# Performance work log

Measured on AMD Instinct MI355X. Metric: run time of the kernel, lower is better.

## Reference

```python
import jax, jax.numpy as jnp
import numpy as np

B, T, D, H, DH, COUT, PRED, K, DFF = 16, 512, 512, 8, 64, 7, 96, 16, 2048
LOW_FREQ = 1
LN_EPS = 1e-5


def _next_fast_len(n):
    while True:
        m = n
        for p in (2, 3, 5):
            while m % p == 0:
                m //= p
        if m == 1:
            return n
        n += 1


def conv1d_fft(f, g, axis=1):
    # FFT cross-correlation, matching torch conv1d_fft (roll + tail slice)
    N = f.shape[axis]
    M = g.shape[axis]
    L = _next_fast_len(N + M - 1)
    Ff = jnp.fft.rfft(f, n=L, axis=axis)
    Fg = jnp.fft.rfft(g, n=L, axis=axis)
    out = jnp.fft.irfft(Ff * jnp.conj(Fg), n=L, axis=axis)
    out = jnp.roll(out, -1, axis=axis)
    return jax.lax.slice_in_dim(out, L - N, L, axis=axis)


def es_weights(sw, T_):
    alpha = jax.nn.sigmoid(sw)                       # (h,1)
    powers = jnp.arange(T_, dtype=jnp.float32)       # (T,)
    init_w = alpha ** (powers + 1.0)                 # (h,T)
    w = (1.0 - alpha) * alpha ** powers[::-1]        # (h,T)
    return init_w.T[None, :, :, None], w.T[None, :, :, None]  # (1,T,h,1)


def exponential_smoothing(values, v0, sw, aux_values=None):
    b, t, h, d = values.shape
    init_w, w = es_weights(sw, t)
    out = init_w * v0 + conv1d_fft(values, w, axis=1)
    if aux_values is not None:
        alpha = jax.nn.sigmoid(sw).reshape(1, 1, h, 1)
        aux_w = w / jnp.maximum(1.0 - alpha, 1e-6) * alpha
        out = out + conv1d_fft(aux_values, aux_w, axis=1)
    return out


def fourier_extrapolate(x, pred_len, k, low_freq=LOW_FREQ):
    b, t, d = x.shape
    x_freq = jnp.fft.rfft(x, axis=1)                 # (b, t//2+1, d)
    hi_end = x_freq.shape[1] - 1 if t % 2 == 0 else x_freq.shape[1]
    x_freq_high = x_freq[:, low_freq:hi_end]
    k_ = k if (k is not None and k < t // 2) else max(1, hi_end - low_freq)
    k_ = min(k_, x_freq_high.shape[1])
    mag = jnp.abs(x_freq_high).transpose(0, 2, 1)    # (b,d,F)
    _, idx = jax.lax.top_k(mag, k_)                  # (b,d,k)
    idx = idx.transpose(0, 2, 1) + low_freq          # (b,k,d)
    x_topk = jnp.take_along_axis(x_freq, idx, axis=1)
    freqs = jnp.fft.rfftfreq(t).astype(jnp.float32)
    f_topk = jnp.take_along_axis(
        jnp.broadcast_to(freqs[None, :, None], (b, freqs.shape[0], d)), idx, axis=1)
    x_ex = jnp.concatenate([x_topk, jnp.conj(x_topk)], axis=1)   # (b,2k,d)
    f_ex = jnp.concatenate([f_topk, -f_topk], axis=1)
    tt = jnp.arange(t + pred_len, dtype=jnp.float32)[None, None, :, None]
    amp = (jnp.abs(x_ex) / t)[:, :, None, :]
    phase = jnp.angle(x_ex)[:, :, None, :]
    x_time = amp * jnp.cos(2.0 * jnp.pi * f_ex[:, :, None, :] * tt + phase)
    return x_time.sum(axis=1)                        # (b, t+pred_len, d)


def layer_norm(x, g, b, eps=LN_EPS):
    mu = x.mean(-1, keepdims=True)
    var = ((x - mu) ** 2).mean(-1, keepdims=True)
    return (x - mu) / jnp.sqrt(var + eps) * g + b


def _forward(res, level, Wi, bi, z0, v0_g, sw_g, Wo, bo, W1, W2,
             g1, b1_ln, g2, b2_ln, Wg, bg, Ws, bs, v0_l, sw_l):
    b, t, _ = res.shape
    # season block
    season = fourier_extrapolate(res, PRED, K)               # (b, t+PRED, d)
    res1 = res - season[:, :t]
    # growth block
    v = (res1 @ Wi.T + bi).reshape(b, t, H, DH)
    v = jnp.concatenate([jnp.broadcast_to(z0[None, None], (b, 1, H, DH)), v], axis=1)
    diffs = v[:, 1:] - v[:, :-1]                             # (b,t,H,DH)
    sm = exponential_smoothing(diffs, v0_g, sw_g)
    gr = jnp.concatenate([jnp.broadcast_to(v0_g, (b, 1, H, DH)), sm], axis=1)
    growth = gr.reshape(b, t + 1, H * DH) @ Wo.T + bo        # (b,t+1,d)
    # residual path
    h = layer_norm(res1 - growth[:, 1:], g1, b1_ln)
    ff = jax.nn.relu(h @ W1.T) @ W2.T
    h = layer_norm(h + ff, g2, b2_ln)
    # level block
    gp = growth[:, 1:t + 1] @ Wg.T + bg                      # (b,t,COUT)
    sp = season[:, :t] @ Ws.T + bs
    es_in = (level - sp)[..., None]                          # (b,t,COUT,1)
    lvl = exponential_smoothing(es_in, v0_l, sw_l, aux_values=gp[..., None])[..., 0]
    return h, lvl, growth, season


def setup_inputs() -> dict:
    key = jax.random.key(0)
    ks = jax.random.split(key, 20)
    s = 0.02
    return {
        "res": jax.random.normal(ks[0], (B, T, D), jnp.float32),
        "level": jax.random.normal(ks[1], (B, T, COUT), jnp.float32),
        "Wi": jax.random.normal(ks[2], (H * DH, D), jnp.float32) * s,
        "bi": jnp.zeros((H * DH,), jnp.float32),
        "z0": jax.random.normal(ks[3], (H, DH), jnp.float32),
        "v0_g": jax.random.normal(ks[4], (1, 1, H, DH), jnp.float32),
        "sw_g": jax.random.normal(ks[5], (H, 1), jnp.float32),
        "Wo": jax.random.normal(ks[6], (D, H * DH), jnp.float32) * s,
        "bo": jnp.zeros((D,), jnp.float32),
        "W1": jax.random.normal(ks[7], (DFF, D), jnp.float32) * s,
        "W2": jax.random.normal(ks[8], (D, DFF), jnp.float32) * s,
        "g1": jnp.ones((D,), jnp.float32),
        "b1_ln": jnp.zeros((D,), jnp.float32),
        "g2": jnp.ones((D,), jnp.float32),
        "b2_ln": jnp.zeros((D,), jnp.float32),
        "Wg": jax.random.normal(ks[9], (COUT, D), jnp.float32) * s,
        "bg": jnp.zeros((COUT,), jnp.float32),
        "Ws": jax.random.normal(ks[10], (COUT, D), jnp.float32) * s,
        "bs": jnp.zeros((COUT,), jnp.float32),
        "v0_l": jax.random.normal(ks[11], (1, 1, COUT, 1), jnp.float32),
        "sw_l": jax.random.normal(ks[12], (COUT, 1), jnp.float32),
    }


def reference(res, level, Wi, bi, z0, v0_g, sw_g, Wo, bo, W1, W2,
              g1, b1_ln, g2, b2_ln, Wg, bg, Ws, bs, v0_l, sw_l):
    return _forward(res, level, Wi, bi, z0, v0_g, sw_g, Wo, bo, W1, W2,
                    g1, b1_ln, g2, b2_ln, Wg, bg, Ws, bs, v0_l, sw_l)
```

## Files before the change

kernel.cpp:

```cpp
#include <hip/hip_runtime.h>
#include <math.h>

#define Bn 16
#define Tn 512
#define Dn 512
#define COUTn 7
#define PREDn 96

using f32x4 = __attribute__((ext_vector_type(4))) float;
using bf16x8 = __attribute__((ext_vector_type(8))) __bf16;

__device__ __forceinline__ unsigned short f2b(float f) {
  unsigned int u = __float_as_uint(f);
  u += 0x7fff + ((u >> 16) & 1);
  return (unsigned short)(u >> 16);
}

__device__ __forceinline__ void gld16(const void* g, void* l) {
  __builtin_amdgcn_global_load_lds(
      (const __attribute__((address_space(1))) void*)g,
      (__attribute__((address_space(3))) void*)l, 16, 0, 0);
}

__global__ __launch_bounds__(256) void cvt_bf16(
    const float* __restrict__ in, unsigned short* __restrict__ out, int n) {
  int i = (blockIdx.x * 256 + threadIdx.x) * 4;
  if (i + 3 < n) {
    float4 v = *reinterpret_cast<const float4*>(&in[i]);
    ushort4 o;
    o.x = f2b(v.x); o.y = f2b(v.y); o.z = f2b(v.z); o.w = f2b(v.w);
    *reinterpret_cast<ushort4*>(&out[i]) = o;
  }
}

__global__ __launch_bounds__(256) void twiddle_init2(
    unsigned short* __restrict__ twc_b, unsigned short* __restrict__ tws_b,
    double* __restrict__ tabw, float* __restrict__ c512,
    float* __restrict__ s512) {
  int idx = blockIdx.x * 256 + threadIdx.x;
  int k = idx >> 9, t = idx & 511;
  int m = (k * t) & 511;
  double ang = (double)m * (M_PI / 256.0);
  twc_b[idx] = f2b((float)cos(ang));
  tws_b[idx] = f2b((float)sin(ang));
  if (idx < 512) {
    double a2 = (double)idx * (M_PI / 256.0);
    c512[idx] = (float)cos(a2);
    s512[idx] = (float)sin(a2);
    tabw[2 * idx] = cos(a2);
    tabw[2 * idx + 1] = -sin(a2);
  }
}

__global__ __launch_bounds__(256) void transpose_cvt(
    const float* __restrict__ res, unsigned short* __restrict__ resT) {
  __shared__ unsigned short tile[64][65];
  int b = blockIdx.z;
  int t0 = blockIdx.y * 64, d0 = blockIdx.x * 64;
  int tid = threadIdx.x;
  int c = tid & 63, r4 = (tid >> 6) * 16;
#pragma unroll
  for (int i = 0; i < 16; ++i) {
    int t = t0 + r4 + i;
    tile[r4 + i][c] = f2b(res[((size_t)(b * 512 + t)) * 512 + d0 + c]);
  }
  __syncthreads();
#pragma unroll
  for (int i = 0; i < 16; ++i) {
    int d = d0 + r4 + i;
    resT[((size_t)(b * 512 + d)) * 512 + t0 + c] = tile[c][r4 + i];
  }
}

__global__ __launch_bounds__(256) void screen_mfma(
    const unsigned short* __restrict__ twc_b,
    const unsigned short* __restrict__ tws_b,
    const unsigned short* __restrict__ resT, float* __restrict__ mag) {
  __shared__ unsigned short lAc[2][2048];
  __shared__ unsigned short lAs[2][2048];
  __shared__ unsigned short lB[2][4096];
  int tid = threadIdx.x;
  int wv = tid >> 6, lane = tid & 63;
  int b = blockIdx.z;
  int k0 = blockIdx.y * 64;
  int d0 = blockIdx.x * 128;

  int rA = wv * 16 + (lane >> 2);
  int rB0 = wv * 32 + (lane >> 2);
  int rB1 = rB0 + 16;
  int kk = (lane & 3) * 8;
  int kkA = kk ^ (((rA >> 1) & 3) << 3);
  int kkB0 = kk ^ (((rB0 >> 1) & 3) << 3);
  int kkB1 = kk ^ (((rB1 >> 1) & 3) << 3);
  const unsigned short* ac = twc_b + (size_t)(k0 + rA) * 512 + kkA;
  const unsigned short* as = tws_b + (size_t)(k0 + rA) * 512 + kkA;
  const unsigned short* bb0 = resT + ((size_t)(b * 512 + d0 + rB0)) * 512 + kkB0;
  const unsigned short* bb1 = resT + ((size_t)(b * 512 + d0 + rB1)) * 512 + kkB1;

  int frow = lane & 15, fk = (lane >> 4) * 8;
  int ia[4], ib[2];
#pragma unroll
  for (int i = 0; i < 4; ++i) {
    int r = i * 16 + frow;
    ia[i] = r * 32 + (fk ^ (((r >> 1) & 3) << 3));
  }
#pragma unroll
  for (int j = 0; j < 2; ++j) {
    int r = wv * 32 + j * 16 + frow;
    ib[j] = r * 32 + (fk ^ (((r >> 1) & 3) << 3));
  }

  f32x4 accR[4][2] = {};
  f32x4 accI[4][2] = {};

  gld16(ac, &lAc[0][wv * 512]);
  gld16(as, &lAs[0][wv * 512]);
  gld16(bb0, &lB[0][wv * 1024]);
  gld16(bb1, &lB[0][wv * 1024 + 512]);
  __syncthreads();

  int cur = 0;
  for (int t = 0; t < 16; ++t) {
    if (t + 1 < 16) {
      int ko = (t + 1) * 32;
      gld16(ac + ko, &lAc[cur ^ 1][wv * 512]);
      gld16(as + ko, &lAs[cur ^ 1][wv * 512]);
      gld16(bb0 + ko, &lB[cur ^ 1][wv * 1024]);
      gld16(bb1 + ko, &lB[cur ^ 1][wv * 1024 + 512]);
    }
    bf16x8 afc[4], afs[4], bw[2];
#pragma unroll
    for (int i = 0; i < 4; ++i) {
      afc[i] = *reinterpret_cast<const bf16x8*>(&lAc[cur][ia[i]]);
      afs[i] = *reinterpret_cast<const bf16x8*>(&lAs[cur][ia[i]]);
    }
#pragma unroll
    for (int j = 0; j < 2; ++j)
      bw[j] = *reinterpret_cast<const bf16x8*>(&lB[cur][ib[j]]);
#pragma unroll
    for (int i = 0; i < 4; ++i)
#pragma unroll
      for (int j = 0; j < 2; ++j) {
        accR[i][j] = __builtin_amdgcn_mfma_f32_16x16x32_bf16(
            afc[i], bw[j], accR[i][j], 0, 0, 0);
        accI[i][j] = __builtin_amdgcn_mfma_f32_16x16x32_bf16(
            afs[i], bw[j], accI[i][j], 0, 0, 0);
      }
    __syncthreads();
    cur ^= 1;
  }

  int ccol = lane & 15, crow4 = (lane >> 4) * 4;
#pragma unroll
  for (int i = 0; i < 4; ++i) {
    int kb = k0 + i * 16 + crow4;
#pragma unroll
    for (int j = 0; j < 2; ++j) {
      int d = d0 + wv * 32 + j * 16 + ccol;
#pragma unroll
      for (int r = 0; r < 4; ++r) {
        float re = accR[i][j][r], im = accI[i][j][r];
        mag[((size_t)(b * 256 + kb + r)) * 512 + d] = re * re + im * im;
      }
    }
  }
}

__global__ __launch_bounds__(64) void cand32(
    const float* __restrict__ mag, int* __restrict__ cand) {
  int blk = blockIdx.x;
  int b = blk >> 9;
  int d = blk & 511;
  int lane = threadIdx.x;
  float m2[4];
#pragma unroll
  for (int i = 0; i < 4; ++i) {
    int k = 1 + lane + 64 * i;
    m2[i] = (k <= 255) ? mag[((size_t)(b * 256 + k)) * 512 + d] : -1.f;
  }
  for (int j = 0; j < 32; ++j) {
    float bm = -2.f; int bk = 1 << 20;
#pragma unroll
    for (int i = 0; i < 4; ++i) {
      int k = 1 + lane + 64 * i;
      if (m2[i] > bm || (m2[i] == bm && k < bk)) { bm = m2[i]; bk = k; }
    }
    for (int o = 32; o > 0; o >>= 1) {
      float om = __shfl_down(bm, o, 64);
      int ok = __shfl_down(bk, o, 64);
      if (om > bm || (om == bm && ok < bk)) { bm = om; bk = ok; }
    }
    bk = __shfl(bk, 0, 64);
    if (lane == 0) cand[((size_t)(b * 32 + j)) * 512 + d] = bk;
#pragma unroll
    for (int i = 0; i < 4; ++i) {
      int k = 1 + lane + 64 * i;
      if (k == bk) m2[i] = -1.f;
    }
  }
}

__global__ __launch_bounds__(512) void refine32(
    const float* __restrict__ res, const int* __restrict__ cand,
    const double* __restrict__ tabw, int* __restrict__ kidx,
    float* __restrict__ cjb, float* __restrict__ sjb) {
  int b = blockIdx.y;
  int d0 = blockIdx.x * 16;
  int tid = threadIdx.x;
  __shared__ float colbuf[512][17];
  for (int idx = tid; idx < 8192; idx += 512) {
    int t = idx >> 4, c = idx & 15;
    colbuf[t][c] = res[((size_t)(b * 512 + t)) * 512 + d0 + c];
  }
  __syncthreads();

  int j = tid & 31, c = tid >> 5;
  int k = cand[((size_t)(b * 32 + j)) * 512 + d0 + c];
  double wr = tabw[2 * k], wi = tabw[2 * k + 1];
  double zr = 1.0, zi = 0.0, ar = 0.0, ai = 0.0;
#pragma unroll 4
  for (int t = 0; t < 512; ++t) {
    double x = (double)colbuf[t][c];
    ar = fma(x, zr, ar);
    ai = fma(x, zi, ai);
    double nzr = fma(zr, wr, -zi * wi);
    double nzi = fma(zr, wi, zi * wr);
    zr = nzr; zi = nzi;
  }
  double m2 = ar * ar + ai * ai;
  float cjv = (float)(ar * (2.0 / 512.0));
  float sjv = (float)(ai * (2.0 / 512.0));
  for (int jo = 0; jo < 16; ++jo) {
    double bm = m2; int bk = k;
#pragma unroll
    for (int o = 16; o > 0; o >>= 1) {
      double om = __shfl_xor(bm, o, 32);
      int ok = __shfl_xor(bk, o, 32);
      if (om > bm || (om == bm && ok < bk)) { bm = om; bk = ok; }
    }
    if (k == bk) {
      size_t o = ((size_t)(b * 16 + jo)) * 512 + d0 + c;
      kidx[o] = k; cjb[o] = cjv; sjb[o] = sjv;
      m2 = -1.0;
    }
  }
}

__global__ __launch_bounds__(512) void synth_kernel(
    const int* __restrict__ kidx, const float* __restrict__ cjb,
    const float* __restrict__ sjb, const float* __restrict__ c512,
    const float* __restrict__ s512, const float* __restrict__ res,
    float* __restrict__ season, unsigned short* __restrict__ res1b) {
  int b = blockIdx.y;
  int t0 = blockIdx.x * 16;
  int d = threadIdx.x;

  __shared__ float ct[512], st[512];
  ct[d] = c512[d];
  st[d] = s512[d];
  __syncthreads();

  int kk[16];
  float cw[16], sw[16];
#pragma unroll
  for (int j = 0; j < 16; ++j) {
    size_t o = ((size_t)(b * 16 + j)) * 512 + d;
    kk[j] = kidx[o];
    cw[j] = cjb[o];
    sw[j] = sjb[o];
  }

  for (int tt = 0; tt < 16; ++tt) {
    int t = t0 + tt;
    if (t >= Tn + PREDn) break;
    float acc = 0.f;
#pragma unroll
    for (int j = 0; j < 16; ++j) {
      int m = (kk[j] * t) & 511;
      acc += cw[j] * ct[m] - sw[j] * st[m];
    }
    season[((size_t)(b * (Tn + PREDn) + t)) * 512 + d] = acc;
    if (t < Tn) {
      size_t o = ((size_t)(b * Tn + t)) * 512 + d;
      res1b[o] = f2b(res[o] - acc);
    }
  }
}

template <int MODE, int BM, int BN>
__global__ __launch_bounds__(256) void gemm_mfma(
    const unsigned short* __restrict__ A, const unsigned short* __restrict__ W,
    const float* __restrict__ bias, float* __restrict__ C,
    unsigned short* __restrict__ Cb, int M, int N, int Kd, int ldk,
    int k0off) {
  constexpr int MF = BM / 32;
  constexpr int NF = BN / 32;
  constexpr int NSA = BM / 64;
  constexpr int NSB = BN / 64;
  __shared__ unsigned short lA[2][BM * 32];
  __shared__ unsigned short lB[2][BN * 32];
  int tid = threadIdx.x;
  int wv = tid >> 6, lane = tid & 63;
  int m0 = blockIdx.x * BM, n0 = blockIdx.y * BN;
  int wr = (wv >> 1) * (BM / 2), wc = (wv & 1) * (BN / 2);
  int kk = (lane & 3) * 8;

  const unsigned short* aptr[NSA];
  const unsigned short* bptr[NSB];
#pragma unroll
  for (int g = 0; g < NSA; ++g) {
    int rA = wv * (BM / 4) + g * 16 + (lane >> 2);
    int kkg = kk ^ (((rA >> 1) & 3) << 3);
    int gm = m0 + rA; if (gm > M - 1) gm = M - 1;
    aptr[g] = A + (size_t)gm * ldk + k0off + kkg;
  }
#pragma unroll
  for (int g = 0; g < NSB; ++g) {
    int rB = wv * (BN / 4) + g * 16 + (lane >> 2);
    int kkg = kk ^ (((rB >> 1) & 3) << 3);
    bptr[g] = W + (size_t)(n0 + rB) * ldk + k0off + kkg;
  }

  int frow = lane & 15, fk = (lane >> 4) * 8;
  int ia[MF], ib[NF];
#pragma unroll
  for (int i = 0; i < MF; ++i) {
    int r = wr + i * 16 + frow;
    ia[i] = r * 32 + (fk ^ (((r >> 1) & 3) << 3));
  }
#pragma unroll
  for (int j = 0; j < NF; ++j) {
    int r = wc + j * 16 + frow;
    ib[j] = r * 32 + (fk ^ (((r >> 1) & 3) << 3));
  }

  f32x4 acc[MF][NF] = {};
  int nk = Kd >> 5;

#pragma unroll
  for (int g = 0; g < NSA; ++g) gld16(aptr[g], &lA[0][wv * BM * 8 + g * 512]);
#pragma unroll
  for (int g = 0; g < NSB; ++g) gld16(bptr[g], &lB[0][wv * BN * 8 + g * 512]);
  __syncthreads();

  int cur = 0;
  for (int t = 0; t < nk; ++t) {
    if (t + 1 < nk) {
      int ko = (t + 1) << 5;
#pragma unroll
      for (int g = 0; g < NSA; ++g)
        gld16(aptr[g] + ko, &lA[cur ^ 1][wv * BM * 8 + g * 512]);
#pragma unroll
      for (int g = 0; g < NSB; ++g)
        gld16(bptr[g] + ko, &lB[cur ^ 1][wv * BN * 8 + g * 512]);
    }
    bf16x8 af[MF], bw[NF];
#pragma unroll
    for (int i = 0; i < MF; ++i)
      af[i] = *reinterpret_cast<const bf16x8*>(&lA[cur][ia[i]]);
#pragma unroll
    for (int j = 0; j < NF; ++j)
      bw[j] = *reinterpret_cast<const bf16x8*>(&lB[cur][ib[j]]);
#pragma unroll
    for (int i = 0; i < MF; ++i)
#pragma unroll
      for (int j = 0; j < NF; ++j)
        acc[i][j] = __builtin_amdgcn_mfma_f32_16x16x32_bf16(
            af[i], bw[j], acc[i][j], 0, 0, 0);
    __syncthreads();
    cur ^= 1;
  }

  int ccol = lane & 15, crow4 = (lane >> 4) * 4;
#pragma unroll
  for (int i = 0; i < MF; ++i) {
    int gm0 = m0 + wr + i * 16 + crow4;
#pragma unroll
    for (int j = 0; j < NF; ++j) {
      int gn = n0 + wc + j * 16 + ccol;
      float bv = 0.f;
      if (MODE == 0) bv = bias[gn];
#pragma unroll
      for (int r = 0; r < 4; ++r) {
        int gm = gm0 + r;
        if (gm < M) {
          size_t o = (size_t)gm * N + gn;
          float v = acc[i][j][r] + bv;
          if (MODE == 1) Cb[o] = f2b(fmaxf(v, 0.f));
          else if (MODE == 2) C[o] += v;
          else C[o] = v;
        }
      }
    }
  }
}

__global__ __launch_bounds__(256) void ema_gA(
    const float* __restrict__ v, const float* __restrict__ z0,
    const float* __restrict__ sw_g, float* __restrict__ tmp,
    float* __restrict__ sumend) {
  int g = blockIdx.x * 256 + threadIdx.x;
  int hd = g & 511;
  int ch = (g >> 9) & 7;
  int b = g >> 12;
  int h = hd >> 6;
  float alpha = 1.f / (1.f + expf(-sw_g[h]));
  float om = 1.f - alpha;
  int t0 = ch * 64;
  float prev = (t0 == 0) ? z0[hd] : v[((size_t)(b * 512 + t0 - 1)) * 512 + hd];
  float s = 0.f;
  for (int i = 0; i < 64; ++i) {
    float cur = v[((size_t)(b * 512 + t0 + i)) * 512 + hd];
    s = alpha * s + om * (cur - prev);
    prev = cur;
    tmp[((size_t)(b * 512 + t0 + i)) * 512 + hd] = s;
  }
  sumend[((size_t)(b * 512 + hd)) * 8 + ch] = s;
}

__global__ __launch_bounds__(256) void ema_gB(
    const float* __restrict__ sumend, const float* __restrict__ v0_g,
    const float* __restrict__ sw_g, float* __restrict__ carry,
    unsigned short* __restrict__ grb) {
  int g = blockIdx.x * 256 + threadIdx.x;
  int hd = g & 511, b = g >> 9, h = hd >> 6;
  float alpha = 1.f / (1.f + expf(-sw_g[h]));
  float A64 = exp2f(64.f * log2f(alpha));
  float cin = v0_g[hd];
  grb[((size_t)(b * 513)) * 512 + hd] = f2b(cin);
  for (int ch = 0; ch < 8; ++ch) {
    carry[((size_t)(b * 512 + hd)) * 8 + ch] = cin;
    cin = A64 * cin + sumend[((size_t)(b * 512 + hd)) * 8 + ch];
  }
}

__global__ __launch_bounds__(256) void ema_gC(
    const float* __restrict__ tmp, const float* __restrict__ carry,
    const float* __restrict__ sw_g, unsigned short* __restrict__ grb) {
  int g = blockIdx.x * 256 + threadIdx.x;
  int hd = g & 511;
  int t = (g >> 9) & 511;
  int b = g >> 18;
  int h = hd >> 6;
  float alpha = 1.f / (1.f + expf(-sw_g[h]));
  int ch = t >> 6, i = t & 63;
  float Ai = exp2f((float)(i + 1) * log2f(alpha));
  float s = tmp[g] + Ai * carry[((size_t)(b * 512 + hd)) * 8 + ch];
  grb[((size_t)(b * 513 + t + 1)) * 512 + hd] = f2b(s);
}

__global__ __launch_bounds__(256) void ln0_kernel(
    const float* __restrict__ res, const float* __restrict__ season,
    const float* __restrict__ growth, const float* __restrict__ g,
    const float* __restrict__ bvec, float* __restrict__ h1,
    unsigned short* __restrict__ h1b) {
  int row = blockIdx.x, b = row >> 9, t = row & 511;
  int tid = threadIdx.x;
  const float* xr = res + (size_t)row * 512;
  const float* sr = season + ((size_t)(b * (Tn + PREDn) + t)) * 512;
  const float* gr = growth + ((size_t)(b * (Tn + 1) + t + 1)) * 512;
  float2 xv = *reinterpret_cast<const float2*>(&xr[tid * 2]);
  float2 sv = *reinterpret_cast<const float2*>(&sr[tid * 2]);
  float2 gv2 = *reinterpret_cast<const float2*>(&gr[tid * 2]);
  float v0 = xv.x - sv.x - gv2.x;
  float v1 = xv.y - sv.y - gv2.y;
  float s1 = v0 + v1;
  float s2 = v0 * v0 + v1 * v1;
  for (int o = 32; o > 0; o >>= 1) {
    s1 += __shfl_down(s1, o, 64);
    s2 += __shfl_down(s2, o, 64);
  }
  __shared__ float r1[4], r2[4];
  __shared__ float mu_s, rstd_s;
  int wv = tid >> 6, ln = tid & 63;
  if (ln == 0) { r1[wv] = s1; r2[wv] = s2; }
  __syncthreads();
  if (tid == 0) {
    float S1 = r1[0] + r1[1] + r1[2] + r1[3];
    float S2 = r2[0] + r2[1] + r2[2] + r2[3];
    float mu = S1 * (1.0f / 512.0f);
    float var = S2 * (1.0f / 512.0f) - mu * mu;
    mu_s = mu;
    rstd_s = rsqrtf(var + 1e-5f);
  }
  __syncthreads();
  float mu = mu_s, rstd = rstd_s;
  float2 gv = *reinterpret_cast<const float2*>(&g[tid * 2]);
  float2 bv = *reinterpret_cast<const float2*>(&bvec[tid * 2]);
  float o0 = (v0 - mu) * rstd * gv.x + bv.x;
  float o1 = (v1 - mu) * rstd * gv.y + bv.y;
  size_t o = (size_t)row * 512 + tid * 2;
  *reinterpret_cast<float2*>(&h1[o]) = make_float2(o0, o1);
  ushort2 hb; hb.x = f2b(o0); hb.y = f2b(o1);
  *reinterpret_cast<ushort2*>(&h1b[o]) = hb;
}

__global__ __launch_bounds__(256) void ln1_kernel(
    const float* __restrict__ X, const float* __restrict__ g,
    const float* __restrict__ bvec, float* __restrict__ out) {
  int row = blockIdx.x;
  int tid = threadIdx.x;
  const float* xr = X + (size_t)row * 512;
  float2 xv = *reinterpret_cast<const float2*>(&xr[tid * 2]);
  float v0 = xv.x, v1 = xv.y;
  float s1 = v0 + v1;
  float s2 = v0 * v0 + v1 * v1;
  for (int o = 32; o > 0; o >>= 1) {
    s1 += __shfl_down(s1, o, 64);
    s2 += __shfl_down(s2, o, 64);
  }
  __shared__ float r1[4], r2[4];
  __shared__ float mu_s, rstd_s;
  int wv = tid >> 6, ln = tid & 63;
  if (ln == 0) { r1[wv] = s1; r2[wv] = s2; }
  __syncthreads();
  if (tid == 0) {
    float S1 = r1[0] + r1[1] + r1[2] + r1[3];
    float S2 = r2[0] + r2[1] + r2[2] + r2[3];
    float mu = S1 * (1.0f / 512.0f);
    float var = S2 * (1.0f / 512.0f) - mu * mu;
    mu_s = mu;
    rstd_s = rsqrtf(var + 1e-5f);
  }
  __syncthreads();
  float mu = mu_s, rstd = rstd_s;
  float2 gv = *reinterpret_cast<const float2*>(&g[tid * 2]);
  float2 bv = *reinterpret_cast<const float2*>(&bvec[tid * 2]);
  float o0 = (v0 - mu) * rstd * gv.x + bv.x;
  float o1 = (v1 - mu) * rstd * gv.y + bv.y;
  *reinterpret_cast<float2*>(&out[(size_t)row * 512 + tid * 2]) =
      make_float2(o0, o1);
}

__global__ __launch_bounds__(64) void proj7_dual(
    const float* __restrict__ growth, const float* __restrict__ season,
    const float* __restrict__ Wg, const float* __restrict__ bg,
    const float* __restrict__ Wse, const float* __restrict__ bs,
    float* __restrict__ gpb, float* __restrict__ spb) {
  int bt = blockIdx.x;
  int which = blockIdx.y;
  int b = bt >> 9;
  int t = bt & 511;
  int lane = threadIdx.x;
  const float* X = which ? season : growth;
  int strB = which ? (Tn + PREDn) : (Tn + 1);
  int off = which ? 0 : 1;
  const float* Wc = which ? Wse : Wg;
  const float* bc = which ? bs : bg;
  float* outp = which ? spb : gpb;
  const float* row = X + ((size_t)(b * strB + off + t)) * 512;
  float x[8];
#pragma unroll
  for (int i = 0; i < 8; ++i) x[i] = row[lane + 64 * i];
#pragma unroll
  for (int c = 0; c < 7; ++c) {
    float s = 0.f;
#pragma unroll
    for (int i = 0; i < 8; ++i) s += x[i] * Wc[c * 512 + lane + 64 * i];
    for (int o = 32; o > 0; o >>= 1) s += __shfl_down(s, o, 64);
    if (lane == 0) outp[((size_t)bt) * 7 + c] = s + bc[c];
  }
}

__global__ __launch_bounds__(256) void lvl_scan(
    const float* __restrict__ level, const float* __restrict__ sp,
    const float* __restrict__ gp, const float* __restrict__ v0_l,
    const float* __restrict__ sw_l, float* __restrict__ out_lvl) {
  int blk = blockIdx.x;
  int b = blk / 7, c = blk % 7;
  int tid = threadIdx.x;
  float alpha = 1.f / (1.f + expf(-sw_l[c]));
  float om = 1.f - alpha;
  size_t i0 = ((size_t)(b * 512 + 2 * tid)) * 7 + c;
  size_t i1 = i0 + 7;
  float u0 = om * (level[i0] - sp[i0]) + alpha * gp[i0];
  float u1 = om * (level[i1] - sp[i1]) + alpha * gp[i1];
  __shared__ float As[256], Us[256];
  As[tid] = alpha * alpha;
  Us[tid] = alpha * u0 + u1;
  __syncthreads();
  for (int off = 1; off < 256; off <<= 1) {
    float Ap = 1.f, Up = 0.f;
    if (tid >= off) { Ap = As[tid - off]; Up = Us[tid - off]; }
    __syncthreads();
    if (tid >= off) {
      float Ac = As[tid], Uc = Us[tid];
      As[tid] = Ac * Ap;
      Us[tid] = Ac * Up + Uc;
    }
    __syncthreads();
  }
  float v0 = v0_l[c];
  float Aex = (tid == 0) ? 1.f : As[tid - 1];
  float Uex = (tid == 0) ? 0.f : Us[tid - 1];
  float sprev = Aex * v0 + Uex;
  float o0 = alpha * sprev + u0;
  float o1 = alpha * o0 + u1;
  out_lvl[i0] = o0;
  out_lvl[i1] = o1;
}

extern "C" void kernel_launch(void* const* d_in, const int* in_sizes, int n_in,
                              void* d_out, int out_size, void* d_ws,
                              size_t ws_size, hipStream_t stream) {
  const float* res = (const float*)d_in[0];
  const float* level = (const float*)d_in[1];
  const float* Wi = (const float*)d_in[2];
  const float* bi = (const float*)d_in[3];
  const float* z0 = (const float*)d_in[4];
  const float* v0_g = (const float*)d_in[5];
  const float* sw_g = (const float*)d_in[6];
  const float* Wo = (const float*)d_in[7];
  const float* bo = (const float*)d_in[8];
  const float* W1 = (const float*)d_in[9];
  const float* W2 = (const float*)d_in[10];
  const float* g1 = (const float*)d_in[11];
  const float* b1 = (const float*)d_in[12];
  const float* g2 = (const float*)d_in[13];
  const float* b2 = (const float*)d_in[14];
  const float* Wg = (const float*)d_in[15];
  const float* bg = (const float*)d_in[16];
  const float* Wse = (const float*)d_in[17];
  const float* bs = (const float*)d_in[18];
  const float* v0_l = (const float*)d_in[19];
  const float* sw_l = (const float*)d_in[20];

  float* out = (float*)d_out;
  float* out_h = out;
  float* out_lvl = out + 4194304;
  float* out_growth = out + 4251648;
  float* out_season = out + 8454144;

  float* wsf = (float*)d_ws;
  unsigned short* res1_b = (unsigned short*)wsf;
  unsigned short* h1_b = (unsigned short*)wsf;
  float* gpb = wsf;
  float* spb = wsf + 57344;
  unsigned short* resT_b = (unsigned short*)(wsf + 2097152);
  float* magb = wsf + 4194304;
  int* candb = (int*)(wsf + 6291456);
  unsigned short* twc_b = (unsigned short*)(wsf + 6553600);
  unsigned short* tws_b = (unsigned short*)(wsf + 6619136);
  float* vbuf = wsf + 2097152;
  unsigned short* grbuf_b = (unsigned short*)(wsf + 6291456);
  float* sumend = wsf + 8392704;
  float* carryb = wsf + 8458240;
  unsigned short* ff1_b = (unsigned short*)(wsf + 2097152);
  double* tabw = (double*)(wsf + 10485760);
  float* c512 = wsf + 10487808;
  float* s512 = wsf + 10488320;
  int* kidx = (int*)(wsf + 10488832);
  float* cjb = wsf + 10619904;
  float* sjb = wsf + 10750976;
  float* tmpb = wsf + 10485760;
  float* h1 = wsf + 10485760;
  unsigned short* Wi_b = (unsigned short*)(wsf + 14680064);
  unsigned short* Wo_b = (unsigned short*)(wsf + 14811136);
  unsigned short* W1_b = (unsigned short*)(wsf + 14942208);
  unsigned short* W2_b = (unsigned short*)(wsf + 15466496);

  hipLaunchKernelGGL(cvt_bf16, dim3(256), dim3(256), 0, stream, Wi, Wi_b, 262144);
  hipLaunchKernelGGL(cvt_bf16, dim3(256), dim3(256), 0, stream, Wo, Wo_b, 262144);
  hipLaunchKernelGGL(cvt_bf16, dim3(1024), dim3(256), 0, stream, W1, W1_b, 1048576);
  hipLaunchKernelGGL(cvt_bf16, dim3(1024), dim3(256), 0, stream, W2, W2_b, 1048576);

  hipLaunchKernelGGL(twiddle_init2, dim3(512), dim3(256), 0, stream,
                     twc_b, tws_b, tabw, c512, s512);
  hipLaunchKernelGGL(transpose_cvt, dim3(8, 8, 16), dim3(256), 0, stream,
                     res, resT_b);
  hipLaunchKernelGGL(screen_mfma, dim3(4, 4, 16), dim3(256), 0, stream,
                     twc_b, tws_b, resT_b, magb);
  hipLaunchKernelGGL(cand32, dim3(8192), dim3(64), 0, stream, magb, candb);
  hipLaunchKernelGGL(refine32, dim3(32, 16), dim3(512), 0, stream,
                     res, candb, tabw, kidx, cjb, sjb);
  hipLaunchKernelGGL(synth_kernel, dim3(38, 16), dim3(512), 0, stream,
                     kidx, cjb, sjb, c512, s512, res, out_season, res1_b);
  hipLaunchKernelGGL((gemm_mfma<0, 64, 128>), dim3(128, 4), dim3(256), 0,
                     stream, res1_b, Wi_b, bi, vbuf, (unsigned short*)nullptr,
                     8192, 512, 512, 512, 0);
  hipLaunchKernelGGL(ema_gA, dim3(256), dim3(256), 0, stream,
                     vbuf, z0, sw_g, tmpb, sumend);
  hipLaunchKernelGGL(ema_gB, dim3(32), dim3(256), 0, stream,
                     sumend, v0_g, sw_g, carryb, grbuf_b);
  hipLaunchKernelGGL(ema_gC, dim3(16384), dim3(256), 0, stream,
                     tmpb, carryb, sw_g, grbuf_b);
  hipLaunchKernelGGL((gemm_mfma<0, 64, 128>), dim3(129, 4), dim3(256), 0,
                     stream, grbuf_b, Wo_b, bo, out_growth,
                     (unsigned short*)nullptr, 8208, 512, 512, 512, 0);
  hipLaunchKernelGGL(ln0_kernel, dim3(Bn * Tn), dim3(256), 0, stream,
                     res, out_season, out_growth, g1, b1, h1, h1_b);
  hipLaunchKernelGGL((gemm_mfma<1, 64, 128>), dim3(128, 16), dim3(256), 0,
                     stream, h1_b, W1_b, (const float*)nullptr,
                     (float*)nullptr, ff1_b, 8192, 2048, 512, 512, 0);
  hipLaunchKernelGGL((gemm_mfma<2, 64, 128>), dim3(128, 4), dim3(256), 0,
                     stream, ff1_b, W2_b, (const float*)nullptr, h1,
                     (unsigned short*)nullptr, 8192, 512, 1024, 2048, 0);
  hipLaunchKernelGGL((gemm_mfma<2, 64, 128>), dim3(128, 4), dim3(256), 0,
                     stream, ff1_b, W2_b, (const float*)nullptr, h1,
                     (unsigned short*)nullptr, 8192, 512, 1024, 2048, 1024);
  hipLaunchKernelGGL(ln1_kernel, dim3(Bn * Tn), dim3(256), 0, stream,
                     h1, g2, b2, out_h);
  hipLaunchKernelGGL(proj7_dual, dim3(Bn * Tn, 2), dim3(64), 0, stream,
                     out_growth, out_season, Wg, bg, Wse, bs, gpb, spb);
  hipLaunchKernelGGL(lvl_scan, dim3(112), dim3(256), 0, stream,
                     level, spb, gpb, v0_l, sw_l, out_lvl);

  (void)in_sizes; (void)n_in; (void)out_size; (void)ws_size;
}
```

Measured before the change: 481.4 us.

## Transpose magnitude layout, pack keys for cand32 top-k, split refine recurrence

The screening kernel now writes squared magnitudes transposed per (b,d) row with float4 stores. cand32 packs each magnitude with its frequency index into one sortable uint key, sorts four keys per lane and runs 32 rounds of wave max-reduction, with four waves per block. This replaces the per-round compare-and-index shuffles and strided loads. refine32 splits the double-precision twiddle recurrence into even and odd chains to shorten the dependency chain. The packed keys drop the low 8 mantissa bits, so near-tie candidates may be ordered differently, and the split recurrence changes rounding slightly.

Result: faster. 444.2 us (-7.7%).

```diff
diff --git a/kernel.cpp b/kernel.cpp
--- a/kernel.cpp
+++ b/kernel.cpp
@@ -20,6 +20,13 @@
   __builtin_amdgcn_global_load_lds(
       (const __attribute__((address_space(1))) void*)g,
       (__attribute__((address_space(3))) void*)l, 16, 0, 0);
+}
+
+__device__ __forceinline__ unsigned int umaxu(unsigned int a, unsigned int b) {
+  return a > b ? a : b;
+}
+__device__ __forceinline__ unsigned int uminu(unsigned int a, unsigned int b) {
+  return a < b ? a : b;
 }
 
 __global__ __launch_bounds__(256) void cvt_bf16(
@@ -75,7 +82,7 @@
 __global__ __launch_bounds__(256) void screen_mfma(
     const unsigned short* __restrict__ twc_b,
     const unsigned short* __restrict__ tws_b,
-    const unsigned short* __restrict__ resT, float* __restrict__ mag) {
+    const unsigned short* __restrict__ resT, float* __restrict__ magT) {
   __shared__ unsigned short lAc[2][2048];
   __shared__ unsigned short lAs[2][2048];
   __shared__ unsigned short lB[2][4096];
@@ -157,47 +164,58 @@
 #pragma unroll
     for (int j = 0; j < 2; ++j) {
       int d = d0 + wv * 32 + j * 16 + ccol;
-#pragma unroll
-      for (int r = 0; r < 4; ++r) {
-        float re = accR[i][j][r], im = accI[i][j][r];
-        mag[((size_t)(b * 256 + kb + r)) * 512 + d] = re * re + im * im;
-      }
-    }
-  }
-}
-
-__global__ __launch_bounds__(64) void cand32(
-    const float* __restrict__ mag, int* __restrict__ cand) {
-  int blk = blockIdx.x;
-  int b = blk >> 9;
-  int d = blk & 511;
-  int lane = threadIdx.x;
-  float m2[4];
-#pragma unroll
-  for (int i = 0; i < 4; ++i) {
-    int k = 1 + lane + 64 * i;
-    m2[i] = (k <= 255) ? mag[((size_t)(b * 256 + k)) * 512 + d] : -1.f;
-  }
+      float4 o;
+      o.x = accR[i][j][0] * accR[i][j][0] + accI[i][j][0] * accI[i][j][0];
+      o.y = accR[i][j][1] * accR[i][j][1] + accI[i][j][1] * accI[i][j][1];
+      o.z = accR[i][j][2] * accR[i][j][2] + accI[i][j][2] * accI[i][j][2];
+      o.w = accR[i][j][3] * accR[i][j][3] + accI[i][j][3] * accI[i][j][3];
+      *reinterpret_cast<float4*>(
+          &magT[((size_t)(b * 512 + d)) * 256 + kb]) = o;
+    }
+  }
+}
+
+__global__ __launch_bounds__(256) void cand32(
+    const float* __restrict__ magT, int* __restrict__ cand) {
+  int gid = blockIdx.x * 4 + (threadIdx.x >> 6);
+  int b = gid >> 9;
+  int d = gid & 511;
+  int lane = threadIdx.x & 63;
+  const float* mrow = magT + ((size_t)(b * 512 + d)) * 256;
+  float4 mv = *reinterpret_cast<const float4*>(&mrow[4 * lane]);
+
+  int kbase = 4 * lane;
+  unsigned int k0 = (kbase + 0 >= 1)
+      ? ((__float_as_uint(mv.x) & 0xFFFFFF00u) | (unsigned)(255 - kbase))
+      : 0u;
+  unsigned int k1 = (__float_as_uint(mv.y) & 0xFFFFFF00u) |
+                    (unsigned)(255 - (kbase + 1));
+  unsigned int k2 = (__float_as_uint(mv.z) & 0xFFFFFF00u) |
+                    (unsigned)(255 - (kbase + 2));
+  unsigned int k3 = (__float_as_uint(mv.w) & 0xFFFFFF00u) |
+                    (unsigned)(255 - (kbase + 3));
+
+  {
+    unsigned int hi, lo;
+    hi = umaxu(k0, k1); lo = uminu(k0, k1); k0 = hi; k1 = lo;
+    hi = umaxu(k2, k3); lo = uminu(k2, k3); k2 = hi; k3 = lo;
+    hi = umaxu(k0, k2); lo = uminu(k0, k2); k0 = hi; k2 = lo;
+    hi = umaxu(k1, k3); lo = uminu(k1, k3); k1 = hi; k3 = lo;
+    hi = umaxu(k1, k2); lo = uminu(k1, k2); k1 = hi; k2 = lo;
+  }
+
+  unsigned int mykeep = 0;
+#pragma unroll
   for (int j = 0; j < 32; ++j) {
-    float bm = -2.f; int bk = 1 << 20;
-#pragma unroll
-    for (int i = 0; i < 4; ++i) {
-      int k = 1 + lane + 64 * i;
-      if (m2[i] > bm || (m2[i] == bm && k < bk)) { bm = m2[i]; bk = k; }
-    }
-    for (int o = 32; o > 0; o >>= 1) {
-      float om = __shfl_down(bm, o, 64);
-      int ok = __shfl_down(bk, o, 64);
-      if (om > bm || (om == bm && ok < bk)) { bm = om; bk = ok; }
-    }
-    bk = __shfl(bk, 0, 64);
-    if (lane == 0) cand[((size_t)(b * 32 + j)) * 512 + d] = bk;
-#pragma unroll
-    for (int i = 0; i < 4; ++i) {
-      int k = 1 + lane + 64 * i;
-      if (k == bk) m2[i] = -1.f;
-    }
-  }
+    unsigned int win = k0;
+#pragma unroll
+    for (int o = 32; o > 0; o >>= 1)
+      win = umaxu(win, (unsigned int)__shfl_xor((int)win, o, 64));
+    if (k0 == win) { k0 = k1; k1 = k2; k2 = k3; k3 = 0u; }
+    if (lane == j) mykeep = win;
+  }
+  if (lane < 32)
+    cand[((size_t)(b * 512 + d)) * 32 + lane] = 255 - (int)(mykeep & 0xFFu);
 }
 
 __global__ __launch_bounds__(512) void refine32(
@@ -215,18 +233,28 @@
   __syncthreads();
 
   int j = tid & 31, c = tid >> 5;
-  int k = cand[((size_t)(b * 32 + j)) * 512 + d0 + c];
+  int k = cand[((size_t)(b * 512 + d0 + c)) * 32 + j];
   double wr = tabw[2 * k], wi = tabw[2 * k + 1];
-  double zr = 1.0, zi = 0.0, ar = 0.0, ai = 0.0;
+  double w2r = wr * wr - wi * wi;
+  double w2i = 2.0 * wr * wi;
+  double zre = 1.0, zie = 0.0;
+  double zro = wr, zio = wi;
+  double are = 0.0, aie = 0.0, aro = 0.0, aio = 0.0;
 #pragma unroll 4
-  for (int t = 0; t < 512; ++t) {
-    double x = (double)colbuf[t][c];
-    ar = fma(x, zr, ar);
-    ai = fma(x, zi, ai);
-    double nzr = fma(zr, wr, -zi * wi);
-    double nzi = fma(zr, wi, zi * wr);
-    zr = nzr; zi = nzi;
-  }
+  for (int t = 0; t < 512; t += 2) {
+    double x0 = (double)colbuf[t][c];
+    double x1 = (double)colbuf[t + 1][c];
+    are = fma(x0, zre, are);
+    aie = fma(x0, zie, aie);
+    aro = fma(x1, zro, aro);
+    aio = fma(x1, zio, aio);
+    double nre = fma(zre, w2r, -zie * w2i);
+    double nie = fma(zre, w2i, zie * w2r);
+    double nro = fma(zro, w2r, -zio * w2i);
+    double nio = fma(zro, w2i, zio * w2r);
+    zre = nre; zie = nie; zro = nro; zio = nio;
+  }
+  double ar = are + aro, ai = aie + aio;
   double m2 = ar * ar + ai * ai;
   float cjv = (float)(ar * (2.0 / 512.0));
   float sjv = (float)(ai * (2.0 / 512.0));
@@ -670,7 +698,7 @@
                      res, resT_b);
   hipLaunchKernelGGL(screen_mfma, dim3(4, 4, 16), dim3(256), 0, stream,
                      twc_b, tws_b, resT_b, magb);
-  hipLaunchKernelGGL(cand32, dim3(8192), dim3(64), 0, stream, magb, candb);
+  hipLaunchKernelGGL(cand32, dim3(2048), dim3(256), 0, stream, magb, candb);
   hipLaunchKernelGGL(refine32, dim3(32, 16), dim3(512), 0, stream,
                      res, candb, tabw, kidx, cjb, sjb);
   hipLaunchKernelGGL(synth_kernel, dim3(38, 16), dim3(512), 0, stream,
```
